# Optimization experiments

Measured on AMD Instinct MI355X. Metric: run time of the kernel, lower is better.

## Reference

```python
import jax, jax.numpy as jnp
import numpy as np
from jax import lax

B, C_IN, T = 64, 40, 8192

def conv1d(x, w, b):
    # x: [B,C,T], w: [O,I,K] (torch Conv1d layout), stride 2, VALID padding
    y = lax.conv_general_dilated(x, w, window_strides=(2,), padding='VALID',
                                 dimension_numbers=('NCH', 'OIH', 'NCH'))
    return y + b[None, :, None]

def avgpool2(x):
    # AvgPool1d(kernel=2, stride=2): pairwise mean, drop trailing odd element
    t2 = x.shape[-1] // 2
    return x[..., :2 * t2].reshape(x.shape[0], x.shape[1], t2, 2).mean(-1)

def setup_inputs():
    key = jax.random.key(0)
    ks = jax.random.split(key, 24)
    def w_init(k, shape, fan_in):
        return jax.random.normal(k, shape, jnp.float32) * (1.0 / np.sqrt(fan_in))
    inp = {}
    inp['x_input'] = jax.random.normal(ks[0], (B, C_IN, T), jnp.float32)
    # per-sample valid lengths in [2048, 8192] so the deep strided stack leaves >=1 frame
    inp['len_mask'] = 2048 + jax.random.randint(ks[1], (B,), 0, T - 2048 + 1, dtype=jnp.int32)
    convs = [(96, C_IN, 10), (96, 96, 5), (96, 96, 5), (96, 96, 5), (96, 96, 5), (96, 96, 5), (128, 96, 3)]
    for i, (o, ci, k) in enumerate(convs):
        inp[f'w{i+1}'] = w_init(ks[2 + 2 * i], (o, ci, k), ci * k)
        inp[f'b{i+1}'] = jnp.zeros((o,), jnp.float32)
    lins = [(128, 128), (64, 128), (5, 64)]
    for i, (o, ci) in enumerate(lins):
        inp[f'lw{i+1}'] = w_init(ks[16 + 2 * i], (o, ci), ci)
        inp[f'lb{i+1}'] = jnp.zeros((o,), jnp.float32)
    return inp

def reference(x_input, len_mask, w1, b1, w2, b2, w3, b3, w4, b4, w5, b5, w6, b6, w7, b7,
              lw1, lb1, lw2, lb2, lw3, lb3):
    # Batched masked equivalent of the per-sample ragged loop: for VALID stride-2 convs,
    # output position j depends only on inputs < valid length when j < valid out-length,
    # so we run batched convs on padded input and track per-sample valid lengths.
    Lv = len_mask.astype(jnp.int32)
    x = jax.nn.relu(conv1d(x_input, w1, b1)); Lv = (Lv - 10) // 2 + 1
    x = jax.nn.relu(conv1d(x, w2, b2));       Lv = (Lv - 5) // 2 + 1
    x = jax.nn.relu(conv1d(x, w3, b3));       Lv = (Lv - 5) // 2 + 1
    # cnn_1d_top (dropout in eval mode = identity)
    x = conv1d(x, w4, b4);        Lv = (Lv - 5) // 2 + 1
    x = jax.nn.relu(avgpool2(x)); Lv = Lv // 2
    x = conv1d(x, w5, b5);        Lv = (Lv - 5) // 2 + 1
    x = jax.nn.relu(avgpool2(x)); Lv = Lv // 2
    x = jax.nn.relu(conv1d(x, w6, b6)); Lv = (Lv - 5) // 2 + 1
    x = jax.nn.relu(conv1d(x, w7, b7)); Lv = (Lv - 3) // 2 + 1
    # AdaptiveMaxPool1d(1) over each sample's valid region
    mask = jnp.arange(x.shape[-1])[None, :] < Lv[:, None]          # [B, T_out]
    x = jnp.max(jnp.where(mask[:, None, :], x, -jnp.inf), axis=-1)  # [B, 128]
    # out1_top MLP head
    h = jax.nn.relu(x @ lw1.T + lb1)
    h = jax.nn.relu(h @ lw2.T + lb2)
    return h @ lw3.T + lb3
```

## Files before the change

### kernel.cpp

```cpp
#include <hip/hip_runtime.h>
#include <hip/hip_bf16.h>
#include <math.h>


typedef __attribute__((ext_vector_type(8))) _Float16 f16x8;
typedef __attribute__((ext_vector_type(4))) float f32x4;

__device__ __forceinline__ unsigned short f2h_bits(float f) {
    union { _Float16 h; unsigned short u; } cv;
    cv.h = (_Float16)f;
    return cv.u;
}

__device__ __forceinline__ void stage16(const void* g, void* l) {
    __builtin_amdgcn_global_load_lds(
        (const __attribute__((address_space(1))) unsigned int*)g,
        (__attribute__((address_space(3))) unsigned int*)l, 16, 0, 0);
}

template<int KP, int CI, int NBLK, bool IN_FP32, bool RELU, bool OUT_F16, bool POOL>
__global__ __launch_bounds__(256)
void conv_mfma9(const unsigned short* __restrict__ xh,
                const unsigned short* __restrict__ wpk,
                const float* __restrict__ bias,
                unsigned short* __restrict__ yh,
                float* __restrict__ yf,
                int Tin, int Tout)
{
    constexpr int CO    = 96;
    constexpr int STEPS = CI * KP / 32;
    constexpr int NCI   = 32 / KP;
    constexpr int RD    = NBLK + KP / 2 + 2;
    constexpr int NTW   = NBLK / 64;
    constexpr int TOT   = NCI * RD;
    constexpr int NIT   = (TOT + 255) / 256;

    __shared__ __align__(16) unsigned short As[2][6144];
    __shared__ unsigned int Bs[2][TOT];

    const int tid  = threadIdx.x;
    const int lane = tid & 63;
    const int wave = tid >> 6;
    const int quad = lane >> 4;
    const int l16  = lane & 15;
    const int wc0  = wave * (NBLK / 4);

    const int nT = (Tout + NBLK - 1) / NBLK;
    const int b  = blockIdx.x / nT;
    const int t0 = (blockIdx.x % nT) * NBLK;

    const float* xf = (const float*)xh;
    const unsigned int* xb = (const unsigned int*)xh + (((size_t)b * CI * Tin) >> 1);
    const int rowd = Tin >> 1;

    auto stageA = [&](int s, int buf) {
        const char* g = (const char*)(wpk + (size_t)s * 6144) + (size_t)lane * 16;
        char* l = (char*)&As[buf][0] + (size_t)lane * 16;
        #pragma unroll
        for (int i = 0; i < 3; ++i) {
            int seg = i * 4 + wave;
            stage16(g + seg * 1024, l + seg * 1024);
        }
    };

    unsigned int breg[NIT];
    auto loadB = [&](int s) {
        const int ci0 = s * NCI;
        #pragma unroll
        for (int it = 0; it < NIT; ++it) {
            int i = tid + it * 256;
            if (i < TOT) {
                int r = i / RD, d = i - r * RD;
                if (IN_FP32) {
                    int e = 2 * (t0 + d);
                    if (e > Tin - 2) e = Tin - 2;
                    const float* src = xf + ((size_t)b * CI + ci0 + r) * Tin + e;
                    float2 v = *(const float2*)src;
                    breg[it] = (unsigned int)f2h_bits(v.x)
                             | ((unsigned int)f2h_bits(v.y) << 16);
                } else {
                    breg[it] = *(xb + (size_t)(ci0 + r) * rowd + t0 + d);
                }
            }
        }
    };
    auto storeB = [&](int buf) {
        #pragma unroll
        for (int it = 0; it < NIT; ++it) {
            int i = tid + it * 256;
            if (i < TOT) Bs[buf][i] = breg[it];
        }
    };

    f32x4 acc[6][NTW];
    #pragma unroll
    for (int mt = 0; mt < 6; ++mt)
        #pragma unroll
        for (int nt = 0; nt < NTW; ++nt) acc[mt][nt] = (f32x4)0.f;

    const int cil = (quad * 8) / KP;
    const int dwo = ((quad * 8) % KP) >> 1;

    loadB(0); storeB(0); stageA(0, 0);
    __syncthreads();

    for (int s = 0; s < STEPS; ++s) {
        const int buf = s & 1;

        if (s + 1 < STEPS) {
            loadB(s + 1);
            stageA(s + 1, buf ^ 1);
        }

        f16x8 Ah[6], Al[6];
        #pragma unroll
        for (int mt = 0; mt < 6; ++mt) {
            Ah[mt] = *(const f16x8*)&As[buf][(mt) * 512 + lane * 8];
            Al[mt] = *(const f16x8*)&As[buf][(6 + mt) * 512 + lane * 8];
        }
        const unsigned int* bp = &Bs[buf][cil * RD + wc0 + l16 + dwo];
        #pragma unroll
        for (int nt = 0; nt < NTW; ++nt) {
            union { unsigned int u[4]; f16x8 v; } Bv;
            #pragma unroll
            for (int p = 0; p < 4; ++p) Bv.u[p] = bp[nt * 16 + p];
            #pragma unroll
            for (int mt = 0; mt < 6; ++mt)
                acc[mt][nt] = __builtin_amdgcn_mfma_f32_16x16x32_f16(Ah[mt], Bv.v, acc[mt][nt], 0, 0, 0);
            #pragma unroll
            for (int mt = 0; mt < 6; ++mt)
                acc[mt][nt] = __builtin_amdgcn_mfma_f32_16x16x32_f16(Al[mt], Bv.v, acc[mt][nt], 0, 0, 0);
        }

        if (s + 1 < STEPS) storeB(buf ^ 1);
        __syncthreads();
    }

    #pragma unroll
    for (int mt = 0; mt < 6; ++mt) {
        #pragma unroll
        for (int r = 0; r < 4; ++r) {
            int o = mt * 16 + quad * 4 + r;
            float bv = bias[o];
            #pragma unroll
            for (int nt = 0; nt < NTW; ++nt) {
                int t = t0 + wc0 + nt * 16 + l16;
                float v = acc[mt][nt][r] + bv;
                if (RELU) v = fmaxf(v, 0.f);
                if (POOL) {
                    float sum = v + __shfl_xor(v, 1, 64);
                    if ((lane & 1) == 0 && t + 1 < Tout) {
                        float pr = fmaxf(0.5f * sum, 0.f);
                        size_t pidx = ((size_t)b * CO + o) * (Tout >> 1) + (t >> 1);
                        if (OUT_F16) yh[pidx] = f2h_bits(pr);
                        else         yf[pidx] = pr;
                    }
                } else if (t < Tout) {
                    size_t oidx = ((size_t)b * CO + o) * Tout + t;
                    if (OUT_F16) yh[oidx] = f2h_bits(v);
                    else         yf[oidx] = v;
                }
            }
        }
    }
}

__device__ __forceinline__ void repack_img(const float* __restrict__ w,
                                           unsigned short* __restrict__ wpk,
                                           int idx, int KP, int KW, int CI)
{
    int j = idx & 7, lane = (idx >> 3) & 63, g = idx >> 9;
    int c = g / 24, r = g % 24;
    int mt = r % 6, sh = r / 6;
    int half = sh & 1, s = sh >> 1;
    int S  = c * 2 + s;
    int kg = S * 32 + (lane >> 4) * 8 + j;
    int o  = mt * 16 + (lane & 15);
    int ci = kg / KP, k = kg % KP;
    float val = (k < KW) ? w[((size_t)o * CI + ci) * KW + k] : 0.f;
    _Float16 hh = (_Float16)val;
    union { _Float16 h; unsigned short u; } cv;
    cv.h = (half == 0) ? hh : (_Float16)(val - (float)hh);
    wpk[idx] = cv.u;
}
__device__ __forceinline__ void repack_okc(const float* __restrict__ w,
                                           float* __restrict__ wr,
                                           int idx, int CI, int K, int CO)
{
    int o = idx % CO; int rem = idx / CO; int k = rem % K; int ci = rem / K;
    wr[idx] = w[((size_t)o * CI + ci) * K + k];
}

__global__ void repack_all(const float* w1, const float* w2, const float* w3,
                           const float* w4, const float* w5, const float* w6,
                           const float* w7,
                           unsigned short* p1, unsigned short* p2,
                           unsigned short* p3, unsigned short* p4,
                           unsigned short* p5, float* r6, float* r7)
{
    int idx = blockIdx.x * 256 + threadIdx.x;
    if (idx < 122880) { repack_img(w1, p1, idx, 16, 10, 40); return; }
    idx -= 122880;
    if (idx < 147456) { repack_img(w2, p2, idx, 8, 5, 96); return; }
    idx -= 147456;
    if (idx < 147456) { repack_img(w3, p3, idx, 8, 5, 96); return; }
    idx -= 147456;
    if (idx < 147456) { repack_img(w4, p4, idx, 8, 5, 96); return; }
    idx -= 147456;
    if (idx < 147456) { repack_img(w5, p5, idx, 8, 5, 96); return; }
    idx -= 147456;
    if (idx < 46080)  { repack_okc(w6, r6, idx, 96, 5, 96); return; }
    idx -= 46080;
    if (idx < 36864)  { repack_okc(w7, r7, idx, 96, 3, 128); return; }
}

__global__ __launch_bounds__(256)
void conv6_k(const float* __restrict__ y5p, const float* __restrict__ w6r,
             const float* __restrict__ b6, float* __restrict__ y6)
{
    __shared__ float s5[96 * 62];
    const int b = blockIdx.x >> 2, ob = blockIdx.x & 3;
    const int tid = threadIdx.x;
    for (int i = tid; i < 96 * 62; i += 256) s5[i] = y5p[(size_t)b * 96 * 62 + i];
    __syncthreads();

    const int wave = __builtin_amdgcn_readfirstlane(tid >> 6);
    const int t = tid & 63;
    if (t < 29) {
        const int o0 = ob * 24 + wave * 6;
        float a[6];
        #pragma unroll
        for (int oo = 0; oo < 6; oo++) a[oo] = 0.f;
        for (int ci = 0; ci < 96; ci++) {
            float xr[5];
            #pragma unroll
            for (int k = 0; k < 5; k++) xr[k] = s5[ci * 62 + 2 * t + k];
            #pragma unroll
            for (int k = 0; k < 5; k++) {
                const float* wp = w6r + (ci * 5 + k) * 96 + o0;
                #pragma unroll
                for (int oo = 0; oo < 6; oo++)
                    a[oo] = fmaf(wp[oo], xr[k], a[oo]);
            }
        }
        #pragma unroll
        for (int oo = 0; oo < 6; oo++)
            y6[((size_t)b * 96 + o0 + oo) * 29 + t] = fmaxf(a[oo] + b6[o0 + oo], 0.f);
    }
}

__global__ __launch_bounds__(256)
void tail2(const float* __restrict__ y6,
           const float* __restrict__ w7r, const float* __restrict__ b7,
           const int* __restrict__ lens,
           const float* __restrict__ lw1, const float* __restrict__ lb1,
           const float* __restrict__ lw2, const float* __restrict__ lb2,
           const float* __restrict__ lw3, const float* __restrict__ lb3,
           float* __restrict__ out)
{
    __shared__ float s6[96 * 29 + 8];
    __shared__ float s7[128 * 14];
    __shared__ float feat[128], h1[128], h2[64];

    const int b = blockIdx.x, tid = threadIdx.x;
    for (int i = tid; i < 96 * 29; i += 256) s6[i] = y6[(size_t)b * 96 * 29 + i];
    __syncthreads();

    const int wave = __builtin_amdgcn_readfirstlane(tid >> 6);
    const int lane = tid & 63;
    const int sub  = lane >> 4;
    const int tl   = lane & 15;
    {
        float a[32];
        #pragma unroll
        for (int oo = 0; oo < 32; oo++) a[oo] = 0.f;
        const int ci0 = sub * 24;
        for (int ci = ci0; ci < ci0 + 24; ci++) {
            float xr[3];
            #pragma unroll
            for (int k = 0; k < 3; k++) xr[k] = s6[ci * 29 + 2 * tl + k];
            #pragma unroll
            for (int k = 0; k < 3; k++) {
                const float* wp = w7r + (ci * 3 + k) * 128 + wave * 32;
                #pragma unroll
                for (int oo = 0; oo < 32; oo++)
                    a[oo] = fmaf(wp[oo], xr[k], a[oo]);
            }
        }
        #pragma unroll
        for (int oo = 0; oo < 32; oo++) {
            float v = a[oo];
            v += __shfl_xor(v, 16, 64);
            v += __shfl_xor(v, 32, 64);
            if (sub == 0 && tl < 14) {
                int o = wave * 32 + oo;
                s7[o * 14 + tl] = fmaxf(v + b7[o], 0.f);
            }
        }
    }
    __syncthreads();

    if (tid < 128) {
        int L = lens[b];
        L = (L - 10) / 2 + 1;
        L = (L - 5) / 2 + 1;
        L = (L - 5) / 2 + 1;
        L = (L - 5) / 2 + 1;
        L = L / 2;
        L = (L - 5) / 2 + 1;
        L = L / 2;
        L = (L - 5) / 2 + 1;
        L = (L - 3) / 2 + 1;
        float m = -INFINITY;
        for (int t = 0; t < L; t++) m = fmaxf(m, s7[tid * 14 + t]);
        feat[tid] = m;
    }
    __syncthreads();

    if (tid < 128) {
        float s = lb1[tid];
        for (int i = 0; i < 128; i++) s = fmaf(lw1[tid * 128 + i], feat[i], s);
        h1[tid] = fmaxf(s, 0.f);
    }
    __syncthreads();
    if (tid < 64) {
        float s = lb2[tid];
        for (int i = 0; i < 128; i++) s = fmaf(lw2[tid * 128 + i], h1[i], s);
        h2[tid] = fmaxf(s, 0.f);
    }
    __syncthreads();
    if (tid < 5) {
        float s = lb3[tid];
        for (int i = 0; i < 64; i++) s = fmaf(lw3[tid * 64 + i], h2[i], s);
        out[b * 5 + tid] = s;
    }
}

extern "C" void kernel_launch(void* const* d_in, const int* in_sizes, int n_in,
                              void* d_out, int out_size, void* d_ws, size_t ws_size,
                              hipStream_t stream)
{
    const float* x    = (const float*)d_in[0];
    const int*   lens = (const int*)  d_in[1];
    const float* w1 = (const float*)d_in[2];   const float* b1 = (const float*)d_in[3];
    const float* w2 = (const float*)d_in[4];   const float* b2 = (const float*)d_in[5];
    const float* w3 = (const float*)d_in[6];   const float* b3 = (const float*)d_in[7];
    const float* w4 = (const float*)d_in[8];   const float* b4 = (const float*)d_in[9];
    const float* w5 = (const float*)d_in[10];  const float* b5 = (const float*)d_in[11];
    const float* w6 = (const float*)d_in[12];  const float* b6 = (const float*)d_in[13];
    const float* w7 = (const float*)d_in[14];  const float* b7 = (const float*)d_in[15];
    const float* lw1 = (const float*)d_in[16]; const float* lb1 = (const float*)d_in[17];
    const float* lw2 = (const float*)d_in[18]; const float* lb2 = (const float*)d_in[19];
    const float* lw3 = (const float*)d_in[20]; const float* lb3 = (const float*)d_in[21];
    float* out = (float*)d_out;
    char*  W   = (char*)d_ws;

    size_t off = 0;
    auto take = [&](size_t bytes) {
        size_t o = off; off = (off + bytes + 255) & ~(size_t)255; return o;
    };
    size_t o_y3h = take(((size_t)64 * 96 * 1020 + 2048) * 2);
    size_t o_y4h = take(((size_t)64 * 96 * 254 + 2048) * 2);
    size_t o_y5p = take((size_t)64 * 96 * 62 * 4 + 1024);
    size_t o_y6  = take((size_t)64 * 96 * 29 * 4);
    size_t o_wp1 = take((size_t)122880 * 2);
    size_t o_wp2 = take((size_t)147456 * 2);
    size_t o_wp3 = take((size_t)147456 * 2);
    size_t o_wp4 = take((size_t)147456 * 2);
    size_t o_wp5 = take((size_t)147456 * 2);
    size_t o_w6r = take((size_t)46080 * 4);
    size_t o_w7r = take((size_t)36864 * 4);
    size_t persist = off;

    auto chunk_bytes = [&](int Bc) -> size_t {
        size_t s = 0;
        s += ((size_t)Bc * 96 * 4092 + 2048) * 2 + 256;
        s += ((size_t)Bc * 96 * 2044 + 2048) * 2 + 256;
        return s;
    };
    int Bc = 64;
    while (Bc > 1 && persist + chunk_bytes(Bc) > ws_size) Bc >>= 1;
    size_t o_y1h = take(((size_t)Bc * 96 * 4092 + 2048) * 2);
    size_t o_y2h = take(((size_t)Bc * 96 * 2044 + 2048) * 2);

    auto US = [&](size_t o) { return (unsigned short*)(W + o); };
    auto FP = [&](size_t o) { return (float*)(W + o); };

    repack_all<<<dim3((795648 + 255) / 256), 256, 0, stream>>>(
        w1, w2, w3, w4, w5, w6, w7,
        US(o_wp1), US(o_wp2), US(o_wp3), US(o_wp4), US(o_wp5),
        FP(o_w6r), FP(o_w7r));

    const int nchunks = 64 / Bc;
    for (int c = 0; c < nchunks; c++) {
        const float* xc = x + (size_t)c * Bc * 40 * 8192;

        conv_mfma9<16, 40, 256, true, true, true, false><<<dim3(Bc * 16), 256, 0, stream>>>(
            (const unsigned short*)xc, US(o_wp1), b1, US(o_y1h), nullptr, 8192, 4092);
        conv_mfma9< 8, 96, 256, false, true, true, false><<<dim3(Bc * 8), 256, 0, stream>>>(
            US(o_y1h), US(o_wp2), b2, US(o_y2h), nullptr, 4092, 2044);
        unsigned short* y3h_c = US(o_y3h) + (size_t)c * Bc * 96 * 1020;
        conv_mfma9< 8, 96, 128, false, true, true, false><<<dim3(Bc * 8), 256, 0, stream>>>(
            US(o_y2h), US(o_wp3), b3, y3h_c, nullptr, 2044, 1020);
    }

    conv_mfma9<8, 96, 128, false, false, true, true><<<dim3(64 * 4), 256, 0, stream>>>(
        US(o_y3h), US(o_wp4), b4, US(o_y4h), nullptr, 1020, 508);

    conv_mfma9<8, 96, 64, false, false, false, true><<<dim3(64 * 2), 256, 0, stream>>>(
        US(o_y4h), US(o_wp5), b5, nullptr, FP(o_y5p), 254, 125);

    conv6_k<<<dim3(256), 256, 0, stream>>>(FP(o_y5p), FP(o_w6r), b6, FP(o_y6));

    tail2<<<dim3(64), 256, 0, stream>>>(
        FP(o_y6), FP(o_w7r), b7, lens, lw1, lb1, lw2, lb2, lw3, lb3, out);
}
```

Before: 465.5 us.

## Pack conv reduction dimension tightly to cut zero-padded kernel taps in MFMA

The implicit-GEMM conv kernel previously padded each channel's kernel width to a power of two (16 for K=10, 8 for K=5), so many MFMA K-slots multiplied zeros. It now packs channels with an effective width of 10 or 6. Each 32-wide K step can then span channel boundaries, so per-lane B offsets are computed per step and the B staging loads a few extra rows. This cuts the MFMA steps and weight bytes by roughly a third to a quarter, at the cost of more index arithmetic and a fully unrolled step loop.

```diff
diff --git a/kernel.cpp b/kernel.cpp
--- a/kernel.cpp
+++ b/kernel.cpp
@@ -18,9 +18,9 @@
         (__attribute__((address_space(3))) unsigned int*)l, 16, 0, 0);
 }
 
-template<int KP, int CI, int NBLK, bool IN_FP32, bool RELU, bool OUT_F16, bool POOL>
+template<int KEFF, int KW, int CI, int NBLK, bool IN_FP32, bool RELU, bool OUT_F16, bool POOL>
 __global__ __launch_bounds__(256)
-void conv_mfma9(const unsigned short* __restrict__ xh,
+void conv_tight(const unsigned short* __restrict__ xh,
                 const unsigned short* __restrict__ wpk,
                 const float* __restrict__ bias,
                 unsigned short* __restrict__ yh,
@@ -28,11 +28,12 @@
                 int Tin, int Tout)
 {
     constexpr int CO    = 96;
-    constexpr int STEPS = CI * KP / 32;
-    constexpr int NCI   = 32 / KP;
-    constexpr int RD    = NBLK + KP / 2 + 2;
+    constexpr int GTOT  = CI * KEFF;
+    constexpr int STEPS = (GTOT + 31) / 32;
+    constexpr int NR    = (KEFF + 29) / KEFF + 1;
+    constexpr int RD    = NBLK + KEFF / 2;
     constexpr int NTW   = NBLK / 64;
-    constexpr int TOT   = NCI * RD;
+    constexpr int TOT   = NR * RD;
     constexpr int NIT   = (TOT + 255) / 256;
 
     __shared__ __align__(16) unsigned short As[2][6144];
@@ -53,9 +54,9 @@
     const unsigned int* xb = (const unsigned int*)xh + (((size_t)b * CI * Tin) >> 1);
     const int rowd = Tin >> 1;
 
-    auto stageA = [&](int s, int buf) {
+    auto stageA = [&](int s, int bufi) {
         const char* g = (const char*)(wpk + (size_t)s * 6144) + (size_t)lane * 16;
-        char* l = (char*)&As[buf][0] + (size_t)lane * 16;
+        char* l = (char*)&As[bufi][0] + (size_t)lane * 16;
         #pragma unroll
         for (int i = 0; i < 3; ++i) {
             int seg = i * 4 + wave;
@@ -65,30 +66,32 @@
 
     unsigned int breg[NIT];
     auto loadB = [&](int s) {
-        const int ci0 = s * NCI;
+        const int cb = (32 * s) / KEFF;
         #pragma unroll
         for (int it = 0; it < NIT; ++it) {
             int i = tid + it * 256;
             if (i < TOT) {
                 int r = i / RD, d = i - r * RD;
+                int ci = cb + r;
+                if (ci > CI - 1) ci = CI - 1;
                 if (IN_FP32) {
                     int e = 2 * (t0 + d);
                     if (e > Tin - 2) e = Tin - 2;
-                    const float* src = xf + ((size_t)b * CI + ci0 + r) * Tin + e;
+                    const float* src = xf + ((size_t)b * CI + ci) * Tin + e;
                     float2 v = *(const float2*)src;
                     breg[it] = (unsigned int)f2h_bits(v.x)
                              | ((unsigned int)f2h_bits(v.y) << 16);
                 } else {
-                    breg[it] = *(xb + (size_t)(ci0 + r) * rowd + t0 + d);
+                    breg[it] = *(xb + (size_t)ci * rowd + t0 + d);
                 }
             }
         }
     };
-    auto storeB = [&](int buf) {
+    auto storeB = [&](int bufi) {
         #pragma unroll
         for (int it = 0; it < NIT; ++it) {
             int i = tid + it * 256;
-            if (i < TOT) Bs[buf][i] = breg[it];
+            if (i < TOT) Bs[bufi][i] = breg[it];
         }
     };
 
@@ -98,12 +101,10 @@
         #pragma unroll
         for (int nt = 0; nt < NTW; ++nt) acc[mt][nt] = (f32x4)0.f;
 
-    const int cil = (quad * 8) / KP;
-    const int dwo = ((quad * 8) % KP) >> 1;
-
     loadB(0); storeB(0); stageA(0, 0);
     __syncthreads();
 
+    #pragma unroll
     for (int s = 0; s < STEPS; ++s) {
         const int buf = s & 1;
 
@@ -118,12 +119,22 @@
             Ah[mt] = *(const f16x8*)&As[buf][(mt) * 512 + lane * 8];
             Al[mt] = *(const f16x8*)&As[buf][(6 + mt) * 512 + lane * 8];
         }
-        const unsigned int* bp = &Bs[buf][cil * RD + wc0 + l16 + dwo];
+
+        const int cb = (32 * s) / KEFF;
+        int offp[4];
+        #pragma unroll
+        for (int p = 0; p < 4; ++p) {
+            unsigned g = (unsigned)(32 * s + quad * 8 + 2 * p);
+            unsigned ci = g / (unsigned)KEFF;
+            unsigned dwo = (g - ci * (unsigned)KEFF) >> 1;
+            offp[p] = ((int)ci - cb) * RD + wc0 + l16 + (int)dwo;
+        }
+
         #pragma unroll
         for (int nt = 0; nt < NTW; ++nt) {
             union { unsigned int u[4]; f16x8 v; } Bv;
             #pragma unroll
-            for (int p = 0; p < 4; ++p) Bv.u[p] = bp[nt * 16 + p];
+            for (int p = 0; p < 4; ++p) Bv.u[p] = Bs[buf][offp[p] + nt * 16];
             #pragma unroll
             for (int mt = 0; mt < 6; ++mt)
                 acc[mt][nt] = __builtin_amdgcn_mfma_f32_16x16x32_f16(Ah[mt], Bv.v, acc[mt][nt], 0, 0, 0);
@@ -176,8 +187,8 @@
     int S  = c * 2 + s;
     int kg = S * 32 + (lane >> 4) * 8 + j;
     int o  = mt * 16 + (lane & 15);
-    int ci = kg / KP, k = kg % KP;
-    float val = (k < KW) ? w[((size_t)o * CI + ci) * KW + k] : 0.f;
+    int ci = kg / KP, k = kg - ci * KP;
+    float val = (ci < CI && k < KW) ? w[((size_t)o * CI + ci) * KW + k] : 0.f;
     _Float16 hh = (_Float16)val;
     union { _Float16 h; unsigned short u; } cv;
     cv.h = (half == 0) ? hh : (_Float16)(val - (float)hh);
@@ -199,16 +210,16 @@
                            unsigned short* p5, float* r6, float* r7)
 {
     int idx = blockIdx.x * 256 + threadIdx.x;
-    if (idx < 122880) { repack_img(w1, p1, idx, 16, 10, 40); return; }
-    idx -= 122880;
-    if (idx < 147456) { repack_img(w2, p2, idx, 8, 5, 96); return; }
-    idx -= 147456;
-    if (idx < 147456) { repack_img(w3, p3, idx, 8, 5, 96); return; }
-    idx -= 147456;
-    if (idx < 147456) { repack_img(w4, p4, idx, 8, 5, 96); return; }
-    idx -= 147456;
-    if (idx < 147456) { repack_img(w5, p5, idx, 8, 5, 96); return; }
-    idx -= 147456;
+    if (idx < 79872)  { repack_img(w1, p1, idx, 10, 10, 40); return; }
+    idx -= 79872;
+    if (idx < 110592) { repack_img(w2, p2, idx, 6, 5, 96); return; }
+    idx -= 110592;
+    if (idx < 110592) { repack_img(w3, p3, idx, 6, 5, 96); return; }
+    idx -= 110592;
+    if (idx < 110592) { repack_img(w4, p4, idx, 6, 5, 96); return; }
+    idx -= 110592;
+    if (idx < 110592) { repack_img(w5, p5, idx, 6, 5, 96); return; }
+    idx -= 110592;
     if (idx < 46080)  { repack_okc(w6, r6, idx, 96, 5, 96); return; }
     idx -= 46080;
     if (idx < 36864)  { repack_okc(w7, r7, idx, 96, 3, 128); return; }
@@ -363,11 +374,11 @@
     size_t o_y4h = take(((size_t)64 * 96 * 254 + 2048) * 2);
     size_t o_y5p = take((size_t)64 * 96 * 62 * 4 + 1024);
     size_t o_y6  = take((size_t)64 * 96 * 29 * 4);
-    size_t o_wp1 = take((size_t)122880 * 2);
-    size_t o_wp2 = take((size_t)147456 * 2);
-    size_t o_wp3 = take((size_t)147456 * 2);
-    size_t o_wp4 = take((size_t)147456 * 2);
-    size_t o_wp5 = take((size_t)147456 * 2);
+    size_t o_wp1 = take((size_t)79872 * 2);
+    size_t o_wp2 = take((size_t)110592 * 2);
+    size_t o_wp3 = take((size_t)110592 * 2);
+    size_t o_wp4 = take((size_t)110592 * 2);
+    size_t o_wp5 = take((size_t)110592 * 2);
     size_t o_w6r = take((size_t)46080 * 4);
     size_t o_w7r = take((size_t)36864 * 4);
     size_t persist = off;
@@ -386,7 +397,7 @@
     auto US = [&](size_t o) { return (unsigned short*)(W + o); };
     auto FP = [&](size_t o) { return (float*)(W + o); };
 
-    repack_all<<<dim3((795648 + 255) / 256), 256, 0, stream>>>(
+    repack_all<<<dim3((605184 + 255) / 256), 256, 0, stream>>>(
         w1, w2, w3, w4, w5, w6, w7,
         US(o_wp1), US(o_wp2), US(o_wp3), US(o_wp4), US(o_wp5),
         FP(o_w6r), FP(o_w7r));
@@ -395,19 +406,19 @@
     for (int c = 0; c < nchunks; c++) {
         const float* xc = x + (size_t)c * Bc * 40 * 8192;
 
-        conv_mfma9<16, 40, 256, true, true, true, false><<<dim3(Bc * 16), 256, 0, stream>>>(
+        conv_tight<10, 10, 40, 256, true, true, true, false><<<dim3(Bc * 16), 256, 0, stream>>>(
             (const unsigned short*)xc, US(o_wp1), b1, US(o_y1h), nullptr, 8192, 4092);
-        conv_mfma9< 8, 96, 256, false, true, true, false><<<dim3(Bc * 8), 256, 0, stream>>>(
+        conv_tight< 6, 5, 96, 256, false, true, true, false><<<dim3(Bc * 8), 256, 0, stream>>>(
             US(o_y1h), US(o_wp2), b2, US(o_y2h), nullptr, 4092, 2044);
         unsigned short* y3h_c = US(o_y3h) + (size_t)c * Bc * 96 * 1020;
-        conv_mfma9< 8, 96, 128, false, true, true, false><<<dim3(Bc * 8), 256, 0, stream>>>(
+        conv_tight< 6, 5, 96, 128, false, true, true, false><<<dim3(Bc * 8), 256, 0, stream>>>(
             US(o_y2h), US(o_wp3), b3, y3h_c, nullptr, 2044, 1020);
     }
 
-    conv_mfma9<8, 96, 128, false, false, true, true><<<dim3(64 * 4), 256, 0, stream>>>(
+    conv_tight<6, 5, 96, 128, false, false, true, true><<<dim3(64 * 4), 256, 0, stream>>>(
         US(o_y3h), US(o_wp4), b4, US(o_y4h), nullptr, 1020, 508);
 
-    conv_mfma9<8, 96, 64, false, false, false, true><<<dim3(64 * 2), 256, 0, stream>>>(
+    conv_tight<6, 5, 96, 64, false, false, false, true><<<dim3(64 * 2), 256, 0, stream>>>(
         US(o_y4h), US(o_wp5), b5, nullptr, FP(o_y5p), 254, 125);
 
     conv6_k<<<dim3(256), 256, 0, stream>>>(FP(o_y5p), FP(o_w6r), b6, FP(o_y6));
```

Result: faster. 443.6 us (-4.7%).
